# Kernel optimization log

Hardware: AMD Instinct MI355X
Metric: run time of the kernel (lower is better)

Reference implementation:

```python
import jax, jax.numpy as jnp
import numpy as np

N = 100000
E = 3200000
IN_DIM = 128
HID = 64
BN_EPS = 1e-5


def _gcn_conv(x, W, b, src, dst, dinv):
    h = x @ W                                      # [N, out]
    coeff = (dinv[src] * dinv[dst])[:, None]       # [E, 1]
    msg = h[src] * coeff                           # gather over edges
    agg = jax.ops.segment_sum(msg, dst, num_segments=N)
    agg = agg + h * (dinv * dinv)[:, None]         # self-loop term
    return agg + b


def setup_inputs() -> dict:
    key = jax.random.key(0)
    ks = jax.random.split(key, 12)
    x = jax.random.normal(ks[0], (N, IN_DIM), dtype=jnp.float32)
    edge_index = jax.random.randint(ks[1], (2, E), 0, N, dtype=jnp.int64)
    s1 = 1.0 / np.sqrt(IN_DIM)
    s2 = 1.0 / np.sqrt(HID)
    W1 = jax.random.uniform(ks[2], (IN_DIM, HID), jnp.float32, -s1, s1)
    b1 = jnp.zeros((HID,), jnp.float32)
    W2 = jax.random.uniform(ks[3], (HID, HID), jnp.float32, -s2, s2)
    b2 = jnp.zeros((HID,), jnp.float32)
    W3 = jax.random.uniform(ks[4], (HID, 1), jnp.float32, -s2, s2)
    b3 = jnp.zeros((1,), jnp.float32)
    g1 = jnp.ones((HID,), jnp.float32)
    beta1 = jnp.zeros((HID,), jnp.float32)
    m1 = 0.1 * jax.random.normal(ks[5], (HID,), jnp.float32)
    v1 = jax.random.uniform(ks[6], (HID,), jnp.float32) + 0.5
    g2 = jnp.ones((HID,), jnp.float32)
    beta2 = jnp.zeros((HID,), jnp.float32)
    m2 = 0.1 * jax.random.normal(ks[7], (HID,), jnp.float32)
    v2 = jax.random.uniform(ks[8], (HID,), jnp.float32) + 0.5
    return {"x": x, "edge_index": edge_index,
            "W1": W1, "b1": b1, "W2": W2, "b2": b2, "W3": W3, "b3": b3,
            "g1": g1, "beta1": beta1, "m1": m1, "v1": v1,
            "g2": g2, "beta2": beta2, "m2": m2, "v2": v2}


def reference(x, edge_index, W1, b1, W2, b2, W3, b3,
              g1, beta1, m1, v1, g2, beta2, m2, v2):
    src, dst = edge_index[0], edge_index[1]
    # degree with self-loops (computed on destination index, PyG convention)
    deg = jax.ops.segment_sum(jnp.ones((E,), jnp.float32), dst, num_segments=N) + 1.0
    dinv = jax.lax.rsqrt(deg)

    def bn(h, g, beta, m, v):
        return (h - m) * jax.lax.rsqrt(v + BN_EPS) * g + beta

    h = _gcn_conv(x, W1, b1, src, dst, dinv)
    h = jax.nn.relu(bn(h, g1, beta1, m1, v1))  # dropout is a no-op in eval
    h = _gcn_conv(h, W2, b2, src, dst, dinv)
    h = jax.nn.relu(bn(h, g2, beta2, m2, v2))
    h = _gcn_conv(h, W3, b3, src, dst, dinv)
    return jax.nn.sigmoid(h)  # [N, 1]
```

## Files before the change

kernel.cpp:

```cpp
#include <hip/hip_runtime.h>
#include <math.h>

#define N_NODES 100000
#define E_EDGES 3200000
#define IN_DIM_ 128
#define HID_ 64
#define BN_EPS_ 1e-5f

#define PB 250
#define CHUNK 12800
#define NBUCK 391
#define BMAX 9600

typedef __attribute__((ext_vector_type(8))) short short8;
typedef __attribute__((ext_vector_type(4))) float f32x4;
typedef __attribute__((ext_vector_type(2))) float f32x2;

__device__ inline ushort f2bf(float f) {
    union { float f; unsigned u; } c; c.f = f;
    unsigned r = c.u + 0x7fff + ((c.u >> 16) & 1);
    return (ushort)(r >> 16);
}
__device__ inline float bf_lo(unsigned p) { union { unsigned u; float f; } c; c.u = p << 16; return c.f; }
__device__ inline float bf_hi(unsigned p) { union { unsigned u; float f; } c; c.u = p & 0xffff0000u; return c.f; }
__device__ inline f32x2 up2(unsigned u) {
    union { unsigned u; float f; } lo, hi;
    lo.u = u << 16; hi.u = u & 0xffff0000u;
    f32x2 r; r.x = lo.f; r.y = hi.f; return r;
}

__global__ __launch_bounds__(512) void passA1_hist(const int* __restrict__ ei,
                                                   int* __restrict__ histPB) {
    __shared__ int hist[NBUCK];
    int t = threadIdx.x, b = blockIdx.x;
    for (int k = t; k < NBUCK; k += 512) hist[k] = 0;
    __syncthreads();
    int e0 = b * CHUNK, e1 = e0 + CHUNK;
    for (int e = e0 + t; e < e1; e += 512) {
        int d = ei[E_EDGES + e];
        atomicAdd(&hist[d >> 8], 1);
    }
    __syncthreads();
    for (int k = t; k < NBUCK; k += 512) histPB[k * PB + b] = hist[k];
}

__global__ __launch_bounds__(256) void scan_rows(int* __restrict__ histPB,
                                                 int* __restrict__ bucket_tot) {
    __shared__ int wsum[4];
    int k = blockIdx.x, t = threadIdx.x, lane = t & 63, wv = t >> 6;
    int v = (t < PB) ? histPB[k * PB + t] : 0;
    int s = v;
#pragma unroll
    for (int off = 1; off < 64; off <<= 1) {
        int u = __shfl_up(s, off, 64);
        if (lane >= off) s += u;
    }
    if (lane == 63) wsum[wv] = s;
    __syncthreads();
    int wbase = 0;
    for (int w = 0; w < wv; w++) wbase += wsum[w];
    if (t < PB) histPB[k * PB + t] = wbase + s - v;
    if (t == 255) bucket_tot[k] = wbase + s;
}

__global__ __launch_bounds__(512) void scan_totals(const int* __restrict__ bucket_tot,
                                                   int* __restrict__ bucket_base,
                                                   int* __restrict__ row_ptr) {
    __shared__ int wsum[8];
    int t = threadIdx.x, lane = t & 63, wv = t >> 6;
    int v = (t < NBUCK) ? bucket_tot[t] : 0;
    int s = v;
#pragma unroll
    for (int off = 1; off < 64; off <<= 1) {
        int u = __shfl_up(s, off, 64);
        if (lane >= off) s += u;
    }
    if (lane == 63) wsum[wv] = s;
    __syncthreads();
    int wbase = 0;
    for (int w = 0; w < wv; w++) wbase += wsum[w];
    if (t < NBUCK) bucket_base[t] = wbase + s - v;
    if (t == 0) {
        bucket_base[NBUCK] = E_EDGES;
        row_ptr[N_NODES] = E_EDGES;
    }
}

__global__ __launch_bounds__(512) void passA2_sorted(const int* __restrict__ ei,
                                                     const int* __restrict__ histPB,
                                                     const int* __restrict__ bucket_base,
                                                     int* __restrict__ ebuf) {
    __shared__ int sorted[CHUNK];
    __shared__ ushort bid[CHUNK];
    __shared__ int cur[NBUCK];
    __shared__ int lbase[NBUCK];
    int t = threadIdx.x, b = blockIdx.x;
    for (int k = t; k < NBUCK; k += 512) cur[k] = 0;
    __syncthreads();
    int e0 = b * CHUNK;
    for (int e = e0 + t; e < e0 + CHUNK; e += 512)
        atomicAdd(&cur[ei[E_EDGES + e] >> 8], 1);
    __syncthreads();
    if (t < 64) {
        int run = 0;
        for (int c0 = 0; c0 < NBUCK; c0 += 64) {
            int idx = c0 + t;
            int v = (idx < NBUCK) ? cur[idx] : 0;
            int s = v;
#pragma unroll
            for (int off = 1; off < 64; off <<= 1) {
                int u = __shfl_up(s, off, 64);
                if (t >= off) s += u;
            }
            if (idx < NBUCK) lbase[idx] = run + s - v;
            run += __shfl(s, 63, 64);
        }
    }
    __syncthreads();
    for (int k = t; k < NBUCK; k += 512) cur[k] = lbase[k];
    __syncthreads();
    for (int e = e0 + t; e < e0 + CHUNK; e += 512) {
        int s = ei[e];
        int d = ei[E_EDGES + e];
        int k = d >> 8;
        int pos = atomicAdd(&cur[k], 1);
        sorted[pos] = s | ((d & 255) << 17);
        bid[pos] = (ushort)k;
    }
    __syncthreads();
    for (int j = t; j < CHUNK; j += 512) {
        int k = bid[j];
        int dest = bucket_base[k] + histPB[k * PB + b] + (j - lbase[k]);
        ebuf[dest] = sorted[j];
    }
}

__global__ __launch_bounds__(256) void passB_sorted(const int* __restrict__ ebuf,
                                                    const int* __restrict__ bucket_base,
                                                    int* __restrict__ row_ptr,
                                                    int* __restrict__ csr_src,
                                                    float* __restrict__ dinv) {
    __shared__ int sorted[BMAX];
    __shared__ int hist[256];
    __shared__ int wsum[4];
    int b = blockIdx.x, t = threadIdx.x, lane = t & 63, wv = t >> 6;
    int base = bucket_base[b], end = bucket_base[b + 1];
    hist[t] = 0;
    __syncthreads();
    for (int k = base + t; k < end; k += 256)
        atomicAdd(&hist[ebuf[k] >> 17], 1);
    __syncthreads();
    int v = hist[t];
    int s = v;
#pragma unroll
    for (int off = 1; off < 64; off <<= 1) {
        int u = __shfl_up(s, off, 64);
        if (lane >= off) s += u;
    }
    if (lane == 63) wsum[wv] = s;
    __syncthreads();
    int wbase = 0;
    for (int w = 0; w < wv; w++) wbase += wsum[w];
    int excl = wbase + s - v;
    int node = b * 256 + t;
    if (node < N_NODES) {
        row_ptr[node] = base + excl;
        dinv[node] = rsqrtf((float)v + 1.0f);
    }
    __syncthreads();
    hist[t] = excl;
    __syncthreads();
    for (int k = base + t; k < end; k += 256) {
        int pv = ebuf[k];
        int pos = atomicAdd(&hist[pv >> 17], 1);
        if (pos < BMAX) sorted[pos] = pv;
        else csr_src[base + pos] = pv & 0x1FFFF;
    }
    __syncthreads();
    int cnt = end - base;
    if (cnt > BMAX) cnt = BMAX;
    for (int j = t; j < cnt; j += 256)
        csr_src[base + j] = sorted[j] & 0x1FFFF;
}

template<int K, bool BF16IN>
__global__ __launch_bounds__(256) void gemm_bf16(const void* __restrict__ Xv,
                                                 const float* __restrict__ W,
                                                 const float* __restrict__ dinv,
                                                 ushort* __restrict__ hs) {
    constexpr int KP = K + 8;
    __shared__ ushort A_lds[64][KP];
    __shared__ ushort Wt_lds[64][KP];
    int t = threadIdx.x;
    long row0 = (long)blockIdx.x * 64;

    for (int i = t; i < K * 16; i += 256) {
        float4 w4 = ((const float4*)W)[i];
        int k = i >> 4, n = (i & 15) * 4;
        Wt_lds[n + 0][k] = f2bf(w4.x);
        Wt_lds[n + 1][k] = f2bf(w4.y);
        Wt_lds[n + 2][k] = f2bf(w4.z);
        Wt_lds[n + 3][k] = f2bf(w4.w);
    }
    if (BF16IN) {
        constexpr int K2 = K / 2;
        const unsigned* X = (const unsigned*)Xv;
        for (int i = t; i < 64 * K2; i += 256) {
            int r = i / K2, c = i % K2;
            unsigned val = 0;
            long row = row0 + r;
            if (row < N_NODES) val = X[row * K2 + c];
            *(unsigned*)&A_lds[r][c * 2] = val;
        }
    } else {
        constexpr int K4 = K / 4;
        const float* X = (const float*)Xv;
        for (int i = t; i < 64 * K4; i += 256) {
            int r = i / K4, c = i % K4;
            float4 val = make_float4(0.f, 0.f, 0.f, 0.f);
            long row = row0 + r;
            if (row < N_NODES) val = ((const float4*)X)[row * K4 + c];
            int cb = c * 4;
            A_lds[r][cb + 0] = f2bf(val.x);
            A_lds[r][cb + 1] = f2bf(val.y);
            A_lds[r][cb + 2] = f2bf(val.z);
            A_lds[r][cb + 3] = f2bf(val.w);
        }
    }
    __syncthreads();

    int w = t >> 6, l = t & 63;
    int m = l & 15, quad = l >> 4;
    f32x4 acc[4];
#pragma unroll
    for (int c = 0; c < 4; c++) acc[c] = (f32x4){0.f, 0.f, 0.f, 0.f};

#pragma unroll
    for (int ch = 0; ch < K / 32; ch++) {
        short8 a = *(const short8*)&A_lds[16 * w + m][32 * ch + 8 * quad];
#pragma unroll
        for (int c = 0; c < 4; c++) {
            short8 b = *(const short8*)&Wt_lds[16 * c + m][32 * ch + 8 * quad];
            acc[c] = __builtin_amdgcn_mfma_f32_16x16x32_bf16(a, b, acc[c], 0, 0, 0);
        }
    }

#pragma unroll
    for (int r = 0; r < 4; r++) {
        long node = row0 + 16 * w + quad * 4 + r;
        if (node <= N_NODES) {
            float dv = (node < N_NODES) ? dinv[node] : 0.f;
#pragma unroll
            for (int c = 0; c < 4; c++)
                hs[node * 64 + 16 * c + m] = f2bf(acc[c][r] * dv);
        }
    }
}

template<bool LAST>
__global__ __launch_bounds__(256) void gather_feat(const int* __restrict__ row_ptr,
                                                   const int* __restrict__ csr_src,
                                                   const ushort* __restrict__ hs,
                                                   const float* __restrict__ dinv,
                                                   const float* __restrict__ b,
                                                   const float* __restrict__ g,
                                                   const float* __restrict__ beta,
                                                   const float* __restrict__ m,
                                                   const float* __restrict__ v,
                                                   unsigned* __restrict__ y,
                                                   const float* __restrict__ W3,
                                                   float* __restrict__ hs3, int n) {
    int i = (blockIdx.x * 256 + threadIdx.x) >> 6;
    if (i >= n) return;
    int l = threadIdx.x & 63;
    int es = l >> 3, fg = l & 7;
    const char* Hb = (const char*)hs;
    unsigned foff = (unsigned)fg << 4;
    unsigned zoff = ((unsigned)N_NODES << 7) + foff;

    f32x2 a01 = {0.f, 0.f}, a23 = {0.f, 0.f}, a45 = {0.f, 0.f}, a67 = {0.f, 0.f};

    if (es == 0) {
        uint4 p = *(const uint4*)(Hb + (((unsigned)i << 7) + foff));
        a01 += up2(p.x); a23 += up2(p.y); a45 += up2(p.z); a67 += up2(p.w);
    }

    int beg = row_ptr[i], end = row_ptr[i + 1];
    int endm1 = end - 1;
    for (int k = beg + es; k < end; k += 32) {
        int c1 = k + 8, c2 = k + 16, c3 = k + 24;
        int s0 = csr_src[k];
        int s1 = csr_src[c1 < end ? c1 : endm1];
        int s2 = csr_src[c2 < end ? c2 : endm1];
        int s3 = csr_src[c3 < end ? c3 : endm1];
        unsigned o0 = ((unsigned)s0 << 7) + foff;
        unsigned o1 = (c1 < end) ? (((unsigned)s1 << 7) + foff) : zoff;
        unsigned o2 = (c2 < end) ? (((unsigned)s2 << 7) + foff) : zoff;
        unsigned o3 = (c3 < end) ? (((unsigned)s3 << 7) + foff) : zoff;
        uint4 p0 = *(const uint4*)(Hb + o0);
        uint4 p1 = *(const uint4*)(Hb + o1);
        uint4 p2 = *(const uint4*)(Hb + o2);
        uint4 p3 = *(const uint4*)(Hb + o3);
        a01 += up2(p0.x); a23 += up2(p0.y); a45 += up2(p0.z); a67 += up2(p0.w);
        a01 += up2(p1.x); a23 += up2(p1.y); a45 += up2(p1.z); a67 += up2(p1.w);
        a01 += up2(p2.x); a23 += up2(p2.y); a45 += up2(p2.z); a67 += up2(p2.w);
        a01 += up2(p3.x); a23 += up2(p3.y); a45 += up2(p3.z); a67 += up2(p3.w);
    }

    float a0 = a01.x, a1 = a01.y, a2 = a23.x, a3 = a23.y;
    float a4 = a45.x, a5 = a45.y, a6 = a67.x, a7 = a67.y;

#pragma unroll
    for (int off = 8; off < 64; off <<= 1) {
        a0 += __shfl_xor(a0, off, 64);
        a1 += __shfl_xor(a1, off, 64);
        a2 += __shfl_xor(a2, off, 64);
        a3 += __shfl_xor(a3, off, 64);
        a4 += __shfl_xor(a4, off, 64);
        a5 += __shfl_xor(a5, off, 64);
        a6 += __shfl_xor(a6, off, 64);
        a7 += __shfl_xor(a7, off, 64);
    }

    float4 bb0 = ((const float4*)b)[fg * 2],    bb1 = ((const float4*)b)[fg * 2 + 1];
    float4 gg0 = ((const float4*)g)[fg * 2],    gg1 = ((const float4*)g)[fg * 2 + 1];
    float4 be0 = ((const float4*)beta)[fg * 2], be1 = ((const float4*)beta)[fg * 2 + 1];
    float4 mm0 = ((const float4*)m)[fg * 2],    mm1 = ((const float4*)m)[fg * 2 + 1];
    float4 vv0 = ((const float4*)v)[fg * 2],    vv1 = ((const float4*)v)[fg * 2 + 1];
    float di = dinv[i];
    float o0 = fmaxf((di * a0 + bb0.x - mm0.x) * (gg0.x * rsqrtf(vv0.x + BN_EPS_)) + be0.x, 0.f);
    float o1 = fmaxf((di * a1 + bb0.y - mm0.y) * (gg0.y * rsqrtf(vv0.y + BN_EPS_)) + be0.y, 0.f);
    float o2 = fmaxf((di * a2 + bb0.z - mm0.z) * (gg0.z * rsqrtf(vv0.z + BN_EPS_)) + be0.z, 0.f);
    float o3 = fmaxf((di * a3 + bb0.w - mm0.w) * (gg0.w * rsqrtf(vv0.w + BN_EPS_)) + be0.w, 0.f);
    float o4 = fmaxf((di * a4 + bb1.x - mm1.x) * (gg1.x * rsqrtf(vv1.x + BN_EPS_)) + be1.x, 0.f);
    float o5 = fmaxf((di * a5 + bb1.y - mm1.y) * (gg1.y * rsqrtf(vv1.y + BN_EPS_)) + be1.y, 0.f);
    float o6 = fmaxf((di * a6 + bb1.z - mm1.z) * (gg1.z * rsqrtf(vv1.z + BN_EPS_)) + be1.z, 0.f);
    float o7 = fmaxf((di * a7 + bb1.w - mm1.w) * (gg1.w * rsqrtf(vv1.w + BN_EPS_)) + be1.w, 0.f);

    if (LAST) {
        float4 w30 = ((const float4*)W3)[fg * 2], w31 = ((const float4*)W3)[fg * 2 + 1];
        float p = o0 * w30.x + o1 * w30.y + o2 * w30.z + o3 * w30.w +
                  o4 * w31.x + o5 * w31.y + o6 * w31.z + o7 * w31.w;
#pragma unroll
        for (int off = 1; off < 8; off <<= 1)
            p += __shfl_xor(p, off, 64);
        if (l == 0) hs3[i] = p * di;
    } else {
        if (es == 0) {
            uint4 pk;
            pk.x = (unsigned)f2bf(o0) | ((unsigned)f2bf(o1) << 16);
            pk.y = (unsigned)f2bf(o2) | ((unsigned)f2bf(o3) << 16);
            pk.z = (unsigned)f2bf(o4) | ((unsigned)f2bf(o5) << 16);
            pk.w = (unsigned)f2bf(o6) | ((unsigned)f2bf(o7) << 16);
            ((uint4*)y)[(long)i * 8 + fg] = pk;
        }
    }
}

__global__ __launch_bounds__(256) void gather3(const int* __restrict__ row_ptr,
                                               const int* __restrict__ csr_src,
                                               const float* __restrict__ hs3,
                                               const float* __restrict__ dinv,
                                               const float* __restrict__ b3,
                                               float* __restrict__ out, int n) {
    int i = blockIdx.x * 256 + threadIdx.x;
    if (i >= n) return;
    int beg = row_ptr[i], end = row_ptr[i + 1];
    float s0 = hs3[i], s1 = 0.f, s2 = 0.f, s3 = 0.f;
    float s4 = 0.f, s5 = 0.f, s6 = 0.f, s7 = 0.f;
    int k = beg;
    for (; k + 8 <= end; k += 8) {
        s0 += hs3[csr_src[k]];
        s1 += hs3[csr_src[k + 1]];
        s2 += hs3[csr_src[k + 2]];
        s3 += hs3[csr_src[k + 3]];
        s4 += hs3[csr_src[k + 4]];
        s5 += hs3[csr_src[k + 5]];
        s6 += hs3[csr_src[k + 6]];
        s7 += hs3[csr_src[k + 7]];
    }
    for (; k < end; k++) s0 += hs3[csr_src[k]];
    float z = dinv[i] * (((s0 + s1) + (s2 + s3)) + ((s4 + s5) + (s6 + s7))) + b3[0];
    out[i] = 1.f / (1.f + expf(-z));
}

extern "C" void kernel_launch(void* const* d_in, const int* in_sizes, int n_in,
                              void* d_out, int out_size, void* d_ws, size_t ws_size,
                              hipStream_t stream) {
    const int N = N_NODES;
    const int E = E_EDGES;

    const float* x   = (const float*)d_in[0];
    const int*   ei  = (const int*)d_in[1];
    const float* W1  = (const float*)d_in[2];
    const float* b1  = (const float*)d_in[3];
    const float* W2  = (const float*)d_in[4];
    const float* b2  = (const float*)d_in[5];
    const float* W3  = (const float*)d_in[6];
    const float* b3  = (const float*)d_in[7];
    const float* g1  = (const float*)d_in[8];
    const float* bt1 = (const float*)d_in[9];
    const float* m1  = (const float*)d_in[10];
    const float* v1  = (const float*)d_in[11];
    const float* g2  = (const float*)d_in[12];
    const float* bt2 = (const float*)d_in[13];
    const float* m2  = (const float*)d_in[14];
    const float* v2  = (const float*)d_in[15];
    float* out = (float*)d_out;

    int*    wsi         = (int*)d_ws;
    float*  dinv        = (float*)wsi;
    float*  hs3         = (float*)(wsi + (long)N);
    int*    row_ptr     = wsi + 2L * N;
    int*    histPB      = wsi + 3L * N + 16;
    int*    bucket_tot  = histPB + NBUCK * PB;
    int*    bucket_base = bucket_tot + 400;
    int*    csr_src     = bucket_base + 400;
    ushort* hsb         = (ushort*)(csr_src + (long)E);
    unsigned* yb        = (unsigned*)(csr_src + (long)E + 32L * (N + 1));
    int*    ebuf        = (int*)hsb;

    passA1_hist<<<PB, 512, 0, stream>>>(ei, histPB);
    scan_rows<<<NBUCK, 256, 0, stream>>>(histPB, bucket_tot);
    scan_totals<<<1, 512, 0, stream>>>(bucket_tot, bucket_base, row_ptr);
    passA2_sorted<<<PB, 512, 0, stream>>>(ei, histPB, bucket_base, ebuf);
    passB_sorted<<<NBUCK, 256, 0, stream>>>(ebuf, bucket_base, row_ptr, csr_src, dinv);

    gemm_bf16<IN_DIM_, false><<<(N + 63) / 64, 256, 0, stream>>>(x, W1, dinv, hsb);
    gather_feat<false><<<N / 4, 256, 0, stream>>>(row_ptr, csr_src, hsb, dinv,
                                                  b1, g1, bt1, m1, v1, yb, W3, hs3, N);
    gemm_bf16<HID_, true><<<(N + 63) / 64, 256, 0, stream>>>(yb, W2, dinv, hsb);
    gather_feat<true><<<N / 4, 256, 0, stream>>>(row_ptr, csr_src, hsb, dinv,
                                                 b2, g2, bt2, m2, v2, yb, W3, hs3, N);
    gather3<<<(N + 255) / 256, 256, 0, stream>>>(row_ptr, csr_src, hs3, dinv, b3, out, N);
}
```

Before: 397.5 us.

## Map eight rows per wave in gather and sort CSR neighbor lists per row

The feature gather now gives each group of 8 lanes its own destination row, so a wave handles 8 rows instead of one. Each lane group loops over its row's neighbors serially, 8 at a time, which removes the cross-lane shuffle reduction and the idle lanes on low-degree rows. A new bitonic sort kernel orders each row's source indices (for degree up to 64) to improve locality of the gathered rows. The cost is an extra kernel launch and sort pass, plus divergence between rows of different degree inside a wave.

```diff
diff --git a/kernel.cpp b/kernel.cpp
--- a/kernel.cpp
+++ b/kernel.cpp
@@ -21,8 +21,6 @@
     unsigned r = c.u + 0x7fff + ((c.u >> 16) & 1);
     return (ushort)(r >> 16);
 }
-__device__ inline float bf_lo(unsigned p) { union { unsigned u; float f; } c; c.u = p << 16; return c.f; }
-__device__ inline float bf_hi(unsigned p) { union { unsigned u; float f; } c; c.u = p & 0xffff0000u; return c.f; }
 __device__ inline f32x2 up2(unsigned u) {
     union { unsigned u; float f; } lo, hi;
     lo.u = u << 16; hi.u = u & 0xffff0000u;
@@ -181,6 +179,119 @@
     if (cnt > BMAX) cnt = BMAX;
     for (int j = t; j < cnt; j += 256)
         csr_src[base + j] = sorted[j] & 0x1FFFF;
+}
+
+__global__ __launch_bounds__(256) void sort_rows(const int* __restrict__ row_ptr,
+                                                 int* __restrict__ csr_src) {
+    int wv = (blockIdx.x * 256 + threadIdx.x) >> 6;
+    int lane = threadIdx.x & 63;
+    if (wv >= N_NODES) return;
+    int beg = row_ptr[wv], end = row_ptr[wv + 1];
+    int deg = end - beg;
+    if (deg <= 1 || deg > 64) return;
+    int val = (lane < deg) ? csr_src[beg + lane] : 0x7FFFFFFF;
+#pragma unroll
+    for (int k = 2; k <= 64; k <<= 1) {
+#pragma unroll
+        for (int j = 32; j > 0; j >>= 1) {
+            if (j >= k) continue;
+            int other = __shfl_xor(val, j, 64);
+            bool lower = (lane & j) == 0;
+            bool asc = (lane & k) == 0;
+            int mn = min(val, other), mx = max(val, other);
+            val = (lower == asc) ? mn : mx;
+        }
+    }
+    if (lane < deg) csr_src[beg + lane] = val;
+}
+
+template<bool LAST>
+__global__ __launch_bounds__(256) void gather_feat(const int* __restrict__ row_ptr,
+                                                   const int* __restrict__ csr_src,
+                                                   const ushort* __restrict__ hs,
+                                                   const float* __restrict__ dinv,
+                                                   const float* __restrict__ b,
+                                                   const float* __restrict__ g,
+                                                   const float* __restrict__ beta,
+                                                   const float* __restrict__ m,
+                                                   const float* __restrict__ v,
+                                                   unsigned* __restrict__ y,
+                                                   const float* __restrict__ W3,
+                                                   float* __restrict__ hs3, int n) {
+    int wave = (blockIdx.x * 256 + threadIdx.x) >> 6;
+    if ((wave << 3) >= n) return;
+    int l = threadIdx.x & 63;
+    int es = l >> 3, fg = l & 7;
+    int i = (wave << 3) + es;
+    bool rowok = i < n;
+    int ic = rowok ? i : (n - 1);
+
+    const char* Hb = (const char*)hs;
+    unsigned foff = (unsigned)fg << 4;
+    unsigned zoff = ((unsigned)N_NODES << 7) + foff;
+
+    f32x2 a01 = {0.f, 0.f}, a23 = {0.f, 0.f}, a45 = {0.f, 0.f}, a67 = {0.f, 0.f};
+
+    {
+        uint4 p = *(const uint4*)(Hb + (((unsigned)ic << 7) + foff));
+        a01 += up2(p.x); a23 += up2(p.y); a45 += up2(p.z); a67 += up2(p.w);
+    }
+
+    int beg = row_ptr[ic], end = row_ptr[ic + 1];
+    for (int k = beg; k < end; k += 8) {
+        unsigned o[8];
+#pragma unroll
+        for (int j = 0; j < 8; j++) {
+            int kj = k + j;
+            int sj = csr_src[kj < end ? kj : k];
+            o[j] = (kj < end) ? (((unsigned)sj << 7) + foff) : zoff;
+        }
+        uint4 p[8];
+#pragma unroll
+        for (int j = 0; j < 8; j++) p[j] = *(const uint4*)(Hb + o[j]);
+#pragma unroll
+        for (int j = 0; j < 8; j++) {
+            a01 += up2(p[j].x); a23 += up2(p[j].y);
+            a45 += up2(p[j].z); a67 += up2(p[j].w);
+        }
+    }
+
+    float a0 = a01.x, a1 = a01.y, a2 = a23.x, a3 = a23.y;
+    float a4 = a45.x, a5 = a45.y, a6 = a67.x, a7 = a67.y;
+
+    float4 bb0 = ((const float4*)b)[fg * 2],    bb1 = ((const float4*)b)[fg * 2 + 1];
+    float4 gg0 = ((const float4*)g)[fg * 2],    gg1 = ((const float4*)g)[fg * 2 + 1];
+    float4 be0 = ((const float4*)beta)[fg * 2], be1 = ((const float4*)beta)[fg * 2 + 1];
+    float4 mm0 = ((const float4*)m)[fg * 2],    mm1 = ((const float4*)m)[fg * 2 + 1];
+    float4 vv0 = ((const float4*)v)[fg * 2],    vv1 = ((const float4*)v)[fg * 2 + 1];
+    float di = dinv[ic];
+    float o0 = fmaxf((di * a0 + bb0.x - mm0.x) * (gg0.x * rsqrtf(vv0.x + BN_EPS_)) + be0.x, 0.f);
+    float o1 = fmaxf((di * a1 + bb0.y - mm0.y) * (gg0.y * rsqrtf(vv0.y + BN_EPS_)) + be0.y, 0.f);
+    float o2 = fmaxf((di * a2 + bb0.z - mm0.z) * (gg0.z * rsqrtf(vv0.z + BN_EPS_)) + be0.z, 0.f);
+    float o3 = fmaxf((di * a3 + bb0.w - mm0.w) * (gg0.w * rsqrtf(vv0.w + BN_EPS_)) + be0.w, 0.f);
+    float o4 = fmaxf((di * a4 + bb1.x - mm1.x) * (gg1.x * rsqrtf(vv1.x + BN_EPS_)) + be1.x, 0.f);
+    float o5 = fmaxf((di * a5 + bb1.y - mm1.y) * (gg1.y * rsqrtf(vv1.y + BN_EPS_)) + be1.y, 0.f);
+    float o6 = fmaxf((di * a6 + bb1.z - mm1.z) * (gg1.z * rsqrtf(vv1.z + BN_EPS_)) + be1.z, 0.f);
+    float o7 = fmaxf((di * a7 + bb1.w - mm1.w) * (gg1.w * rsqrtf(vv1.w + BN_EPS_)) + be1.w, 0.f);
+
+    if (LAST) {
+        float4 w30 = ((const float4*)W3)[fg * 2], w31 = ((const float4*)W3)[fg * 2 + 1];
+        float p = o0 * w30.x + o1 * w30.y + o2 * w30.z + o3 * w30.w +
+                  o4 * w31.x + o5 * w31.y + o6 * w31.z + o7 * w31.w;
+#pragma unroll
+        for (int off = 1; off < 8; off <<= 1)
+            p += __shfl_xor(p, off, 64);
+        if (fg == 0 && rowok) hs3[i] = p * di;
+    } else {
+        if (rowok) {
+            uint4 pk;
+            pk.x = (unsigned)f2bf(o0) | ((unsigned)f2bf(o1) << 16);
+            pk.y = (unsigned)f2bf(o2) | ((unsigned)f2bf(o3) << 16);
+            pk.z = (unsigned)f2bf(o4) | ((unsigned)f2bf(o5) << 16);
+            pk.w = (unsigned)f2bf(o6) | ((unsigned)f2bf(o7) << 16);
+            ((uint4*)y)[(long)i * 8 + fg] = pk;
+        }
+    }
 }
 
 template<int K, bool BF16IN>
@@ -253,106 +364,6 @@
 #pragma unroll
             for (int c = 0; c < 4; c++)
                 hs[node * 64 + 16 * c + m] = f2bf(acc[c][r] * dv);
-        }
-    }
-}
-
-template<bool LAST>
-__global__ __launch_bounds__(256) void gather_feat(const int* __restrict__ row_ptr,
-                                                   const int* __restrict__ csr_src,
-                                                   const ushort* __restrict__ hs,
-                                                   const float* __restrict__ dinv,
-                                                   const float* __restrict__ b,
-                                                   const float* __restrict__ g,
-                                                   const float* __restrict__ beta,
-                                                   const float* __restrict__ m,
-                                                   const float* __restrict__ v,
-                                                   unsigned* __restrict__ y,
-                                                   const float* __restrict__ W3,
-                                                   float* __restrict__ hs3, int n) {
-    int i = (blockIdx.x * 256 + threadIdx.x) >> 6;
-    if (i >= n) return;
-    int l = threadIdx.x & 63;
-    int es = l >> 3, fg = l & 7;
-    const char* Hb = (const char*)hs;
-    unsigned foff = (unsigned)fg << 4;
-    unsigned zoff = ((unsigned)N_NODES << 7) + foff;
-
-    f32x2 a01 = {0.f, 0.f}, a23 = {0.f, 0.f}, a45 = {0.f, 0.f}, a67 = {0.f, 0.f};
-
-    if (es == 0) {
-        uint4 p = *(const uint4*)(Hb + (((unsigned)i << 7) + foff));
-        a01 += up2(p.x); a23 += up2(p.y); a45 += up2(p.z); a67 += up2(p.w);
-    }
-
-    int beg = row_ptr[i], end = row_ptr[i + 1];
-    int endm1 = end - 1;
-    for (int k = beg + es; k < end; k += 32) {
-        int c1 = k + 8, c2 = k + 16, c3 = k + 24;
-        int s0 = csr_src[k];
-        int s1 = csr_src[c1 < end ? c1 : endm1];
-        int s2 = csr_src[c2 < end ? c2 : endm1];
-        int s3 = csr_src[c3 < end ? c3 : endm1];
-        unsigned o0 = ((unsigned)s0 << 7) + foff;
-        unsigned o1 = (c1 < end) ? (((unsigned)s1 << 7) + foff) : zoff;
-        unsigned o2 = (c2 < end) ? (((unsigned)s2 << 7) + foff) : zoff;
-        unsigned o3 = (c3 < end) ? (((unsigned)s3 << 7) + foff) : zoff;
-        uint4 p0 = *(const uint4*)(Hb + o0);
-        uint4 p1 = *(const uint4*)(Hb + o1);
-        uint4 p2 = *(const uint4*)(Hb + o2);
-        uint4 p3 = *(const uint4*)(Hb + o3);
-        a01 += up2(p0.x); a23 += up2(p0.y); a45 += up2(p0.z); a67 += up2(p0.w);
-        a01 += up2(p1.x); a23 += up2(p1.y); a45 += up2(p1.z); a67 += up2(p1.w);
-        a01 += up2(p2.x); a23 += up2(p2.y); a45 += up2(p2.z); a67 += up2(p2.w);
-        a01 += up2(p3.x); a23 += up2(p3.y); a45 += up2(p3.z); a67 += up2(p3.w);
-    }
-
-    float a0 = a01.x, a1 = a01.y, a2 = a23.x, a3 = a23.y;
-    float a4 = a45.x, a5 = a45.y, a6 = a67.x, a7 = a67.y;
-
-#pragma unroll
-    for (int off = 8; off < 64; off <<= 1) {
-        a0 += __shfl_xor(a0, off, 64);
-        a1 += __shfl_xor(a1, off, 64);
-        a2 += __shfl_xor(a2, off, 64);
-        a3 += __shfl_xor(a3, off, 64);
-        a4 += __shfl_xor(a4, off, 64);
-        a5 += __shfl_xor(a5, off, 64);
-        a6 += __shfl_xor(a6, off, 64);
-        a7 += __shfl_xor(a7, off, 64);
-    }
-
-    float4 bb0 = ((const float4*)b)[fg * 2],    bb1 = ((const float4*)b)[fg * 2 + 1];
-    float4 gg0 = ((const float4*)g)[fg * 2],    gg1 = ((const float4*)g)[fg * 2 + 1];
-    float4 be0 = ((const float4*)beta)[fg * 2], be1 = ((const float4*)beta)[fg * 2 + 1];
-    float4 mm0 = ((const float4*)m)[fg * 2],    mm1 = ((const float4*)m)[fg * 2 + 1];
-    float4 vv0 = ((const float4*)v)[fg * 2],    vv1 = ((const float4*)v)[fg * 2 + 1];
-    float di = dinv[i];
-    float o0 = fmaxf((di * a0 + bb0.x - mm0.x) * (gg0.x * rsqrtf(vv0.x + BN_EPS_)) + be0.x, 0.f);
-    float o1 = fmaxf((di * a1 + bb0.y - mm0.y) * (gg0.y * rsqrtf(vv0.y + BN_EPS_)) + be0.y, 0.f);
-    float o2 = fmaxf((di * a2 + bb0.z - mm0.z) * (gg0.z * rsqrtf(vv0.z + BN_EPS_)) + be0.z, 0.f);
-    float o3 = fmaxf((di * a3 + bb0.w - mm0.w) * (gg0.w * rsqrtf(vv0.w + BN_EPS_)) + be0.w, 0.f);
-    float o4 = fmaxf((di * a4 + bb1.x - mm1.x) * (gg1.x * rsqrtf(vv1.x + BN_EPS_)) + be1.x, 0.f);
-    float o5 = fmaxf((di * a5 + bb1.y - mm1.y) * (gg1.y * rsqrtf(vv1.y + BN_EPS_)) + be1.y, 0.f);
-    float o6 = fmaxf((di * a6 + bb1.z - mm1.z) * (gg1.z * rsqrtf(vv1.z + BN_EPS_)) + be1.z, 0.f);
-    float o7 = fmaxf((di * a7 + bb1.w - mm1.w) * (gg1.w * rsqrtf(vv1.w + BN_EPS_)) + be1.w, 0.f);
-
-    if (LAST) {
-        float4 w30 = ((const float4*)W3)[fg * 2], w31 = ((const float4*)W3)[fg * 2 + 1];
-        float p = o0 * w30.x + o1 * w30.y + o2 * w30.z + o3 * w30.w +
-                  o4 * w31.x + o5 * w31.y + o6 * w31.z + o7 * w31.w;
-#pragma unroll
-        for (int off = 1; off < 8; off <<= 1)
-            p += __shfl_xor(p, off, 64);
-        if (l == 0) hs3[i] = p * di;
-    } else {
-        if (es == 0) {
-            uint4 pk;
-            pk.x = (unsigned)f2bf(o0) | ((unsigned)f2bf(o1) << 16);
-            pk.y = (unsigned)f2bf(o2) | ((unsigned)f2bf(o3) << 16);
-            pk.z = (unsigned)f2bf(o4) | ((unsigned)f2bf(o5) << 16);
-            pk.w = (unsigned)f2bf(o6) | ((unsigned)f2bf(o7) << 16);
-            ((uint4*)y)[(long)i * 8 + fg] = pk;
         }
     }
 }
@@ -425,12 +436,13 @@
     scan_totals<<<1, 512, 0, stream>>>(bucket_tot, bucket_base, row_ptr);
     passA2_sorted<<<PB, 512, 0, stream>>>(ei, histPB, bucket_base, ebuf);
     passB_sorted<<<NBUCK, 256, 0, stream>>>(ebuf, bucket_base, row_ptr, csr_src, dinv);
+    sort_rows<<<(N + 3) / 4, 256, 0, stream>>>(row_ptr, csr_src);
 
     gemm_bf16<IN_DIM_, false><<<(N + 63) / 64, 256, 0, stream>>>(x, W1, dinv, hsb);
-    gather_feat<false><<<N / 4, 256, 0, stream>>>(row_ptr, csr_src, hsb, dinv,
-                                                  b1, g1, bt1, m1, v1, yb, W3, hs3, N);
+    gather_feat<false><<<(N + 31) / 32, 256, 0, stream>>>(row_ptr, csr_src, hsb, dinv,
+                                                          b1, g1, bt1, m1, v1, yb, W3, hs3, N);
     gemm_bf16<HID_, true><<<(N + 63) / 64, 256, 0, stream>>>(yb, W2, dinv, hsb);
-    gather_feat<true><<<N / 4, 256, 0, stream>>>(row_ptr, csr_src, hsb, dinv,
-                                                 b2, g2, bt2, m2, v2, yb, W3, hs3, N);
+    gather_feat<true><<<(N + 31) / 32, 256, 0, stream>>>(row_ptr, csr_src, hsb, dinv,
+                                                         b2, g2, bt2, m2, v2, yb, W3, hs3, N);
     gather3<<<(N + 255) / 256, 256, 0, stream>>>(row_ptr, csr_src, hs3, dinv, b3, out, N);
 }
```

After: 409.3 us. 3.0% more time.

## Split gather into four feature-slice passes over padded CSR rows

Applied to the files above, without the earlier changes.

The hidden features are stored as four column slices of 16 bf16 values each, and each aggregation runs as four separate gather kernels, one per slice. Each slice table (about 3.2 MB) is small enough to stay in cache during the random neighbour gathers. CSR rows are padded to multiples of 8 with a dummy zero node, which removes bounds checks and tail loops. Node degrees now come from a separate global atomic histogram, adding kernels and per-slice launch overhead plus 32-byte-granular gathers that may waste bandwidth.

```diff
diff --git a/kernel.cpp b/kernel.cpp
--- a/kernel.cpp
+++ b/kernel.cpp
@@ -11,6 +11,7 @@
 #define CHUNK 12800
 #define NBUCK 391
 #define BMAX 9600
+#define SUB (N_NODES + 1)
 
 typedef __attribute__((ext_vector_type(8))) short short8;
 typedef __attribute__((ext_vector_type(4))) float f32x4;
@@ -21,8 +22,6 @@
     unsigned r = c.u + 0x7fff + ((c.u >> 16) & 1);
     return (ushort)(r >> 16);
 }
-__device__ inline float bf_lo(unsigned p) { union { unsigned u; float f; } c; c.u = p << 16; return c.f; }
-__device__ inline float bf_hi(unsigned p) { union { unsigned u; float f; } c; c.u = p & 0xffff0000u; return c.f; }
 __device__ inline f32x2 up2(unsigned u) {
     union { unsigned u; float f; } lo, hi;
     lo.u = u << 16; hi.u = u & 0xffff0000u;
@@ -30,9 +29,12 @@
 }
 
 __global__ __launch_bounds__(512) void passA1_hist(const int* __restrict__ ei,
-                                                   int* __restrict__ histPB) {
+                                                   int* __restrict__ histPB,
+                                                   int* __restrict__ deg) {
     __shared__ int hist[NBUCK];
     int t = threadIdx.x, b = blockIdx.x;
+    int g = b * 512 + t;
+    if (g < N_NODES) deg[g] = 0;
     for (int k = t; k < NBUCK; k += 512) hist[k] = 0;
     __syncthreads();
     int e0 = b * CHUNK, e1 = e0 + CHUNK;
@@ -42,6 +44,13 @@
     }
     __syncthreads();
     for (int k = t; k < NBUCK; k += 512) histPB[k * PB + b] = hist[k];
+}
+
+__global__ __launch_bounds__(256) void deg_hist(const int* __restrict__ ei,
+                                                int* __restrict__ deg) {
+    int stride = gridDim.x * 256;
+    for (int e = blockIdx.x * 256 + threadIdx.x; e < E_EDGES; e += stride)
+        atomicAdd(&deg[ei[E_EDGES + e]], 1);
 }
 
 __global__ __launch_bounds__(256) void scan_rows(int* __restrict__ histPB,
@@ -63,26 +72,51 @@
     if (t == 255) bucket_tot[k] = wbase + s;
 }
 
-__global__ __launch_bounds__(512) void scan_totals(const int* __restrict__ bucket_tot,
-                                                   int* __restrict__ bucket_base,
-                                                   int* __restrict__ row_ptr) {
-    __shared__ int wsum[8];
+__global__ __launch_bounds__(256) void pad_tot_k(const int* __restrict__ deg,
+                                                 int* __restrict__ bucket_ptot,
+                                                 float* __restrict__ dinv) {
+    __shared__ int wsum[4];
+    int b = blockIdx.x, t = threadIdx.x, lane = t & 63, wv = t >> 6;
+    int node = b * 256 + t;
+    int d = (node < N_NODES) ? deg[node] : 0;
+    if (node < N_NODES) dinv[node] = rsqrtf((float)d + 1.0f);
+    int pd = (d + 7) & ~7;
+#pragma unroll
+    for (int off = 1; off < 64; off <<= 1) pd += __shfl_xor(pd, off, 64);
+    if (lane == 0) wsum[wv] = pd;
+    __syncthreads();
+    if (t == 0) bucket_ptot[b] = wsum[0] + wsum[1] + wsum[2] + wsum[3];
+}
+
+__global__ __launch_bounds__(512) void scan_totals2(const int* __restrict__ bucket_tot,
+                                                    const int* __restrict__ bucket_ptot,
+                                                    int* __restrict__ bucket_base,
+                                                    int* __restrict__ bucket_pbase,
+                                                    int* __restrict__ row_ptr,
+                                                    float* __restrict__ hs3) {
+    __shared__ int wsA[8], wsB[8];
     int t = threadIdx.x, lane = t & 63, wv = t >> 6;
-    int v = (t < NBUCK) ? bucket_tot[t] : 0;
-    int s = v;
+    int va = (t < NBUCK) ? bucket_tot[t] : 0;
+    int vb = (t < NBUCK) ? bucket_ptot[t] : 0;
+    int sa = va, sb = vb;
 #pragma unroll
     for (int off = 1; off < 64; off <<= 1) {
-        int u = __shfl_up(s, off, 64);
-        if (lane >= off) s += u;
-    }
-    if (lane == 63) wsum[wv] = s;
-    __syncthreads();
-    int wbase = 0;
-    for (int w = 0; w < wv; w++) wbase += wsum[w];
-    if (t < NBUCK) bucket_base[t] = wbase + s - v;
+        int ua = __shfl_up(sa, off, 64);
+        int ub = __shfl_up(sb, off, 64);
+        if (lane >= off) { sa += ua; sb += ub; }
+    }
+    if (lane == 63) { wsA[wv] = sa; wsB[wv] = sb; }
+    __syncthreads();
+    int wa = 0, wb = 0;
+    for (int w = 0; w < wv; w++) { wa += wsA[w]; wb += wsB[w]; }
+    if (t < NBUCK) {
+        bucket_base[t]  = wa + sa - va;
+        bucket_pbase[t] = wb + sb - vb;
+    }
+    if (t == NBUCK - 1) row_ptr[N_NODES] = wb + sb;
     if (t == 0) {
         bucket_base[NBUCK] = E_EDGES;
-        row_ptr[N_NODES] = E_EDGES;
+        hs3[N_NODES] = 0.f;
     }
 }
 
@@ -137,128 +171,54 @@
 
 __global__ __launch_bounds__(256) void passB_sorted(const int* __restrict__ ebuf,
                                                     const int* __restrict__ bucket_base,
+                                                    const int* __restrict__ bucket_pbase,
+                                                    const int* __restrict__ deg,
                                                     int* __restrict__ row_ptr,
-                                                    int* __restrict__ csr_src,
-                                                    float* __restrict__ dinv) {
+                                                    int* __restrict__ csr_src) {
     __shared__ int sorted[BMAX];
-    __shared__ int hist[256];
-    __shared__ int wsum[4];
+    __shared__ int ucur[256];
+    __shared__ int ubeg[256];
+    __shared__ int pbeg[256];
+    __shared__ int wsA[4], wsB[4];
     int b = blockIdx.x, t = threadIdx.x, lane = t & 63, wv = t >> 6;
     int base = bucket_base[b], end = bucket_base[b + 1];
-    hist[t] = 0;
-    __syncthreads();
-    for (int k = base + t; k < end; k += 256)
-        atomicAdd(&hist[ebuf[k] >> 17], 1);
-    __syncthreads();
-    int v = hist[t];
-    int s = v;
+    int pbase = bucket_pbase[b];
+    int node = b * 256 + t;
+    int d = (node < N_NODES) ? deg[node] : 0;
+    int pd = (d + 7) & ~7;
+    int sa = d, sb = pd;
 #pragma unroll
     for (int off = 1; off < 64; off <<= 1) {
-        int u = __shfl_up(s, off, 64);
-        if (lane >= off) s += u;
-    }
-    if (lane == 63) wsum[wv] = s;
-    __syncthreads();
-    int wbase = 0;
-    for (int w = 0; w < wv; w++) wbase += wsum[w];
-    int excl = wbase + s - v;
-    int node = b * 256 + t;
-    if (node < N_NODES) {
-        row_ptr[node] = base + excl;
-        dinv[node] = rsqrtf((float)v + 1.0f);
-    }
-    __syncthreads();
-    hist[t] = excl;
+        int ua = __shfl_up(sa, off, 64);
+        int ub = __shfl_up(sb, off, 64);
+        if (lane >= off) { sa += ua; sb += ub; }
+    }
+    if (lane == 63) { wsA[wv] = sa; wsB[wv] = sb; }
+    __syncthreads();
+    int wa = 0, wb = 0;
+    for (int w = 0; w < wv; w++) { wa += wsA[w]; wb += wsB[w]; }
+    int uex = wa + sa - d, pex = wb + sb - pd;
+    ubeg[t] = uex; pbeg[t] = pex; ucur[t] = uex;
+    if (node < N_NODES) row_ptr[node] = pbase + pex;
     __syncthreads();
     for (int k = base + t; k < end; k += 256) {
         int pv = ebuf[k];
-        int pos = atomicAdd(&hist[pv >> 17], 1);
+        int pos = atomicAdd(&ucur[pv >> 17], 1);
         if (pos < BMAX) sorted[pos] = pv;
-        else csr_src[base + pos] = pv & 0x1FFFF;
-    }
-    __syncthreads();
-    int cnt = end - base;
-    if (cnt > BMAX) cnt = BMAX;
-    for (int j = t; j < cnt; j += 256)
-        csr_src[base + j] = sorted[j] & 0x1FFFF;
-}
-
-template<int K, bool BF16IN>
-__global__ __launch_bounds__(256) void gemm_bf16(const void* __restrict__ Xv,
-                                                 const float* __restrict__ W,
-                                                 const float* __restrict__ dinv,
-                                                 ushort* __restrict__ hs) {
-    constexpr int KP = K + 8;
-    __shared__ ushort A_lds[64][KP];
-    __shared__ ushort Wt_lds[64][KP];
-    int t = threadIdx.x;
-    long row0 = (long)blockIdx.x * 64;
-
-    for (int i = t; i < K * 16; i += 256) {
-        float4 w4 = ((const float4*)W)[i];
-        int k = i >> 4, n = (i & 15) * 4;
-        Wt_lds[n + 0][k] = f2bf(w4.x);
-        Wt_lds[n + 1][k] = f2bf(w4.y);
-        Wt_lds[n + 2][k] = f2bf(w4.z);
-        Wt_lds[n + 3][k] = f2bf(w4.w);
-    }
-    if (BF16IN) {
-        constexpr int K2 = K / 2;
-        const unsigned* X = (const unsigned*)Xv;
-        for (int i = t; i < 64 * K2; i += 256) {
-            int r = i / K2, c = i % K2;
-            unsigned val = 0;
-            long row = row0 + r;
-            if (row < N_NODES) val = X[row * K2 + c];
-            *(unsigned*)&A_lds[r][c * 2] = val;
-        }
-    } else {
-        constexpr int K4 = K / 4;
-        const float* X = (const float*)Xv;
-        for (int i = t; i < 64 * K4; i += 256) {
-            int r = i / K4, c = i % K4;
-            float4 val = make_float4(0.f, 0.f, 0.f, 0.f);
-            long row = row0 + r;
-            if (row < N_NODES) val = ((const float4*)X)[row * K4 + c];
-            int cb = c * 4;
-            A_lds[r][cb + 0] = f2bf(val.x);
-            A_lds[r][cb + 1] = f2bf(val.y);
-            A_lds[r][cb + 2] = f2bf(val.z);
-            A_lds[r][cb + 3] = f2bf(val.w);
-        }
-    }
-    __syncthreads();
-
-    int w = t >> 6, l = t & 63;
-    int m = l & 15, quad = l >> 4;
-    f32x4 acc[4];
-#pragma unroll
-    for (int c = 0; c < 4; c++) acc[c] = (f32x4){0.f, 0.f, 0.f, 0.f};
-
-#pragma unroll
-    for (int ch = 0; ch < K / 32; ch++) {
-        short8 a = *(const short8*)&A_lds[16 * w + m][32 * ch + 8 * quad];
-#pragma unroll
-        for (int c = 0; c < 4; c++) {
-            short8 b = *(const short8*)&Wt_lds[16 * c + m][32 * ch + 8 * quad];
-            acc[c] = __builtin_amdgcn_mfma_f32_16x16x32_bf16(a, b, acc[c], 0, 0, 0);
-        }
-    }
-
-#pragma unroll
-    for (int r = 0; r < 4; r++) {
-        long node = row0 + 16 * w + quad * 4 + r;
-        if (node <= N_NODES) {
-            float dv = (node < N_NODES) ? dinv[node] : 0.f;
-#pragma unroll
-            for (int c = 0; c < 4; c++)
-                hs[node * 64 + 16 * c + m] = f2bf(acc[c][r] * dv);
-        }
-    }
-}
-
-template<bool LAST>
-__global__ __launch_bounds__(256) void gather_feat(const int* __restrict__ row_ptr,
+    }
+    __syncthreads();
+    for (int r = wv; r < 256; r += 4) {
+        int nd = b * 256 + r;
+        int d2 = (nd < N_NODES) ? deg[nd] : 0;
+        int pd2 = (d2 + 7) & ~7;
+        int ub = ubeg[r], pb = pbeg[r];
+        for (int c = lane; c < pd2; c += 64)
+            csr_src[pbase + pb + c] = (c < d2) ? (sorted[ub + c] & 0x1FFFF) : N_NODES;
+    }
+}
+
+template<bool LAST, int P>
+__global__ __launch_bounds__(256) void gather_pass(const int* __restrict__ row_ptr,
                                                    const int* __restrict__ csr_src,
                                                    const ushort* __restrict__ hs,
                                                    const float* __restrict__ dinv,
@@ -274,85 +234,134 @@
     if (i >= n) return;
     int l = threadIdx.x & 63;
     int es = l >> 3, fg = l & 7;
-    const char* Hb = (const char*)hs;
-    unsigned foff = (unsigned)fg << 4;
-    unsigned zoff = ((unsigned)N_NODES << 7) + foff;
-
-    f32x2 a01 = {0.f, 0.f}, a23 = {0.f, 0.f}, a45 = {0.f, 0.f}, a67 = {0.f, 0.f};
-
-    if (es == 0) {
-        uint4 p = *(const uint4*)(Hb + (((unsigned)i << 7) + foff));
-        a01 += up2(p.x); a23 += up2(p.y); a45 += up2(p.z); a67 += up2(p.w);
-    }
-
-    int beg = row_ptr[i], end = row_ptr[i + 1];
-    int endm1 = end - 1;
-    for (int k = beg + es; k < end; k += 32) {
-        int c1 = k + 8, c2 = k + 16, c3 = k + 24;
-        int s0 = csr_src[k];
-        int s1 = csr_src[c1 < end ? c1 : endm1];
-        int s2 = csr_src[c2 < end ? c2 : endm1];
-        int s3 = csr_src[c3 < end ? c3 : endm1];
-        unsigned o0 = ((unsigned)s0 << 7) + foff;
-        unsigned o1 = (c1 < end) ? (((unsigned)s1 << 7) + foff) : zoff;
-        unsigned o2 = (c2 < end) ? (((unsigned)s2 << 7) + foff) : zoff;
-        unsigned o3 = (c3 < end) ? (((unsigned)s3 << 7) + foff) : zoff;
-        uint4 p0 = *(const uint4*)(Hb + o0);
-        uint4 p1 = *(const uint4*)(Hb + o1);
-        uint4 p2 = *(const uint4*)(Hb + o2);
-        uint4 p3 = *(const uint4*)(Hb + o3);
-        a01 += up2(p0.x); a23 += up2(p0.y); a45 += up2(p0.z); a67 += up2(p0.w);
-        a01 += up2(p1.x); a23 += up2(p1.y); a45 += up2(p1.z); a67 += up2(p1.w);
-        a01 += up2(p2.x); a23 += up2(p2.y); a45 += up2(p2.z); a67 += up2(p2.w);
-        a01 += up2(p3.x); a23 += up2(p3.y); a45 += up2(p3.z); a67 += up2(p3.w);
-    }
-
-    float a0 = a01.x, a1 = a01.y, a2 = a23.x, a3 = a23.y;
-    float a4 = a45.x, a5 = a45.y, a6 = a67.x, a7 = a67.y;
+
+    const unsigned* T = (const unsigned*)hs + (long)P * SUB * 8;
+
+    f32x2 acc = {0.f, 0.f};
+    if (es == 0) acc += up2(T[(unsigned)i * 8 + fg]);
+
+    int pbeg = row_ptr[i], pend = row_ptr[i + 1];
+    const int* cs = csr_src + pbeg;
+    int nb8 = (pend - pbeg) >> 3;
+    int k = es;
+    int full = nb8 >> 2;
+    for (int t = 0; t < full; t++, k += 32) {
+        int s0 = cs[k], s1 = cs[k + 8], s2 = cs[k + 16], s3 = cs[k + 24];
+        unsigned u0 = T[(unsigned)s0 * 8 + fg];
+        unsigned u1 = T[(unsigned)s1 * 8 + fg];
+        unsigned u2 = T[(unsigned)s2 * 8 + fg];
+        unsigned u3 = T[(unsigned)s3 * 8 + fg];
+        acc += up2(u0); acc += up2(u1); acc += up2(u2); acc += up2(u3);
+    }
+    for (int rem = nb8 & 3; rem > 0; rem--, k += 8) {
+        int s = cs[k];
+        acc += up2(T[(unsigned)s * 8 + fg]);
+    }
 
 #pragma unroll
     for (int off = 8; off < 64; off <<= 1) {
-        a0 += __shfl_xor(a0, off, 64);
-        a1 += __shfl_xor(a1, off, 64);
-        a2 += __shfl_xor(a2, off, 64);
-        a3 += __shfl_xor(a3, off, 64);
-        a4 += __shfl_xor(a4, off, 64);
-        a5 += __shfl_xor(a5, off, 64);
-        a6 += __shfl_xor(a6, off, 64);
-        a7 += __shfl_xor(a7, off, 64);
-    }
-
-    float4 bb0 = ((const float4*)b)[fg * 2],    bb1 = ((const float4*)b)[fg * 2 + 1];
-    float4 gg0 = ((const float4*)g)[fg * 2],    gg1 = ((const float4*)g)[fg * 2 + 1];
-    float4 be0 = ((const float4*)beta)[fg * 2], be1 = ((const float4*)beta)[fg * 2 + 1];
-    float4 mm0 = ((const float4*)m)[fg * 2],    mm1 = ((const float4*)m)[fg * 2 + 1];
-    float4 vv0 = ((const float4*)v)[fg * 2],    vv1 = ((const float4*)v)[fg * 2 + 1];
+        acc.x += __shfl_xor(acc.x, off, 64);
+        acc.y += __shfl_xor(acc.y, off, 64);
+    }
+
+    float2 bb = ((const float2*)b)[P * 8 + fg];
+    float2 gg = ((const float2*)g)[P * 8 + fg];
+    float2 be = ((const float2*)beta)[P * 8 + fg];
+    float2 mm = ((const float2*)m)[P * 8 + fg];
+    float2 vv = ((const float2*)v)[P * 8 + fg];
     float di = dinv[i];
-    float o0 = fmaxf((di * a0 + bb0.x - mm0.x) * (gg0.x * rsqrtf(vv0.x + BN_EPS_)) + be0.x, 0.f);
-    float o1 = fmaxf((di * a1 + bb0.y - mm0.y) * (gg0.y * rsqrtf(vv0.y + BN_EPS_)) + be0.y, 0.f);
-    float o2 = fmaxf((di * a2 + bb0.z - mm0.z) * (gg0.z * rsqrtf(vv0.z + BN_EPS_)) + be0.z, 0.f);
-    float o3 = fmaxf((di * a3 + bb0.w - mm0.w) * (gg0.w * rsqrtf(vv0.w + BN_EPS_)) + be0.w, 0.f);
-    float o4 = fmaxf((di * a4 + bb1.x - mm1.x) * (gg1.x * rsqrtf(vv1.x + BN_EPS_)) + be1.x, 0.f);
-    float o5 = fmaxf((di * a5 + bb1.y - mm1.y) * (gg1.y * rsqrtf(vv1.y + BN_EPS_)) + be1.y, 0.f);
-    float o6 = fmaxf((di * a6 + bb1.z - mm1.z) * (gg1.z * rsqrtf(vv1.z + BN_EPS_)) + be1.z, 0.f);
-    float o7 = fmaxf((di * a7 + bb1.w - mm1.w) * (gg1.w * rsqrtf(vv1.w + BN_EPS_)) + be1.w, 0.f);
+    float o0 = fmaxf((di * acc.x + bb.x - mm.x) * (gg.x * rsqrtf(vv.x + BN_EPS_)) + be.x, 0.f);
+    float o1 = fmaxf((di * acc.y + bb.y - mm.y) * (gg.y * rsqrtf(vv.y + BN_EPS_)) + be.y, 0.f);
 
     if (LAST) {
-        float4 w30 = ((const float4*)W3)[fg * 2], w31 = ((const float4*)W3)[fg * 2 + 1];
-        float p = o0 * w30.x + o1 * w30.y + o2 * w30.z + o3 * w30.w +
-                  o4 * w31.x + o5 * w31.y + o6 * w31.z + o7 * w31.w;
+        float2 w3 = ((const float2*)W3)[P * 8 + fg];
+        float p = o0 * w3.x + o1 * w3.y;
 #pragma unroll
         for (int off = 1; off < 8; off <<= 1)
             p += __shfl_xor(p, off, 64);
-        if (l == 0) hs3[i] = p * di;
+        if (l == 0) {
+            float prev = (P == 0) ? 0.f : hs3[i];
+            float now = prev + p;
+            hs3[i] = (P == 3) ? now * di : now;
+        }
     } else {
         if (es == 0) {
-            uint4 pk;
-            pk.x = (unsigned)f2bf(o0) | ((unsigned)f2bf(o1) << 16);
-            pk.y = (unsigned)f2bf(o2) | ((unsigned)f2bf(o3) << 16);
-            pk.z = (unsigned)f2bf(o4) | ((unsigned)f2bf(o5) << 16);
-            pk.w = (unsigned)f2bf(o6) | ((unsigned)f2bf(o7) << 16);
-            ((uint4*)y)[(long)i * 8 + fg] = pk;
+            unsigned pk = (unsigned)f2bf(o0) | ((unsigned)f2bf(o1) << 16);
+            y[(unsigned)i * 32 + P * 8 + fg] = pk;
+        }
+    }
+}
+
+template<int K, bool BF16IN>
+__global__ __launch_bounds__(256) void gemm_bf16(const void* __restrict__ Xv,
+                                                 const float* __restrict__ W,
+                                                 const float* __restrict__ dinv,
+                                                 ushort* __restrict__ hs) {
+    constexpr int KP = K + 8;
+    __shared__ ushort A_lds[64][KP];
+    __shared__ ushort Wt_lds[64][KP];
+    int t = threadIdx.x;
+    long row0 = (long)blockIdx.x * 64;
+
+    for (int i = t; i < K * 16; i += 256) {
+        float4 w4 = ((const float4*)W)[i];
+        int k = i >> 4, n = (i & 15) * 4;
+        Wt_lds[n + 0][k] = f2bf(w4.x);
+        Wt_lds[n + 1][k] = f2bf(w4.y);
+        Wt_lds[n + 2][k] = f2bf(w4.z);
+        Wt_lds[n + 3][k] = f2bf(w4.w);
+    }
+    if (BF16IN) {
+        constexpr int K2 = K / 2;
+        const unsigned* X = (const unsigned*)Xv;
+        for (int i = t; i < 64 * K2; i += 256) {
+            int r = i / K2, c = i % K2;
+            unsigned val = 0;
+            long row = row0 + r;
+            if (row < N_NODES) val = X[row * K2 + c];
+            *(unsigned*)&A_lds[r][c * 2] = val;
+        }
+    } else {
+        constexpr int K4 = K / 4;
+        const float* X = (const float*)Xv;
+        for (int i = t; i < 64 * K4; i += 256) {
+            int r = i / K4, c = i % K4;
+            float4 val = make_float4(0.f, 0.f, 0.f, 0.f);
+            long row = row0 + r;
+            if (row < N_NODES) val = ((const float4*)X)[row * K4 + c];
+            int cb = c * 4;
+            A_lds[r][cb + 0] = f2bf(val.x);
+            A_lds[r][cb + 1] = f2bf(val.y);
+            A_lds[r][cb + 2] = f2bf(val.z);
+            A_lds[r][cb + 3] = f2bf(val.w);
+        }
+    }
+    __syncthreads();
+
+    int w = t >> 6, l = t & 63;
+    int m = l & 15, quad = l >> 4;
+    f32x4 acc[4];
+#pragma unroll
+    for (int c = 0; c < 4; c++) acc[c] = (f32x4){0.f, 0.f, 0.f, 0.f};
+
+#pragma unroll
+    for (int ch = 0; ch < K / 32; ch++) {
+        short8 a = *(const short8*)&A_lds[16 * w + m][32 * ch + 8 * quad];
+#pragma unroll
+        for (int c = 0; c < 4; c++) {
+            short8 b = *(const short8*)&Wt_lds[16 * c + m][32 * ch + 8 * quad];
+            acc[c] = __builtin_amdgcn_mfma_f32_16x16x32_bf16(a, b, acc[c], 0, 0, 0);
+        }
+    }
+
+#pragma unroll
+    for (int r = 0; r < 4; r++) {
+        long node = row0 + 16 * w + quad * 4 + r;
+        if (node <= N_NODES) {
+            float dv = (node < N_NODES) ? dinv[node] : 0.f;
+#pragma unroll
+            for (int c = 0; c < 4; c++)
+                hs[((long)c * SUB + node) * 16 + m] = f2bf(acc[c][r] * dv);
         }
     }
 }
@@ -368,8 +377,7 @@
     int beg = row_ptr[i], end = row_ptr[i + 1];
     float s0 = hs3[i], s1 = 0.f, s2 = 0.f, s3 = 0.f;
     float s4 = 0.f, s5 = 0.f, s6 = 0.f, s7 = 0.f;
-    int k = beg;
-    for (; k + 8 <= end; k += 8) {
+    for (int k = beg; k + 8 <= end; k += 8) {
         s0 += hs3[csr_src[k]];
         s1 += hs3[csr_src[k + 1]];
         s2 += hs3[csr_src[k + 2]];
@@ -379,7 +387,6 @@
         s6 += hs3[csr_src[k + 6]];
         s7 += hs3[csr_src[k + 7]];
     }
-    for (; k < end; k++) s0 += hs3[csr_src[k]];
     float z = dinv[i] * (((s0 + s1) + (s2 + s3)) + ((s4 + s5) + (s6 + s7))) + b3[0];
     out[i] = 1.f / (1.f + expf(-z));
 }
@@ -388,7 +395,6 @@
                               void* d_out, int out_size, void* d_ws, size_t ws_size,
                               hipStream_t stream) {
     const int N = N_NODES;
-    const int E = E_EDGES;
 
     const float* x   = (const float*)d_in[0];
     const int*   ei  = (const int*)d_in[1];
@@ -408,29 +414,50 @@
     const float* v2  = (const float*)d_in[15];
     float* out = (float*)d_out;
 
-    int*    wsi         = (int*)d_ws;
-    float*  dinv        = (float*)wsi;
-    float*  hs3         = (float*)(wsi + (long)N);
-    int*    row_ptr     = wsi + 2L * N;
-    int*    histPB      = wsi + 3L * N + 16;
-    int*    bucket_tot  = histPB + NBUCK * PB;
-    int*    bucket_base = bucket_tot + 400;
-    int*    csr_src     = bucket_base + 400;
-    ushort* hsb         = (ushort*)(csr_src + (long)E);
-    unsigned* yb        = (unsigned*)(csr_src + (long)E + 32L * (N + 1));
-    int*    ebuf        = (int*)hsb;
-
-    passA1_hist<<<PB, 512, 0, stream>>>(ei, histPB);
+    int*    wsi          = (int*)d_ws;
+    float*  dinv         = (float*)wsi;
+    float*  hs3          = (float*)(wsi + (long)N);
+    int*    row_ptr      = wsi + 2L * N + 16;
+    int*    deg          = row_ptr + N + 16;
+    int*    histPB       = deg + N + 16;
+    int*    bucket_tot   = histPB + NBUCK * PB;
+    int*    bucket_base  = bucket_tot + 400;
+    int*    bucket_ptot  = bucket_base + 400;
+    int*    bucket_pbase = bucket_ptot + 400;
+    ushort* hsb          = (ushort*)(bucket_pbase + 402);
+    unsigned* yb         = (unsigned*)((int*)(void*)hsb + 32L * SUB);
+    int*    csr_src      = (int*)yb + 32L * N;
+    int*    ebuf         = (int*)(void*)hsb;
+
+    passA1_hist<<<PB, 512, 0, stream>>>(ei, histPB, deg);
+    deg_hist<<<1024, 256, 0, stream>>>(ei, deg);
     scan_rows<<<NBUCK, 256, 0, stream>>>(histPB, bucket_tot);
-    scan_totals<<<1, 512, 0, stream>>>(bucket_tot, bucket_base, row_ptr);
+    pad_tot_k<<<NBUCK, 256, 0, stream>>>(deg, bucket_ptot, dinv);
+    scan_totals2<<<1, 512, 0, stream>>>(bucket_tot, bucket_ptot, bucket_base,
+                                        bucket_pbase, row_ptr, hs3);
     passA2_sorted<<<PB, 512, 0, stream>>>(ei, histPB, bucket_base, ebuf);
-    passB_sorted<<<NBUCK, 256, 0, stream>>>(ebuf, bucket_base, row_ptr, csr_src, dinv);
+    passB_sorted<<<NBUCK, 256, 0, stream>>>(ebuf, bucket_base, bucket_pbase,
+                                            deg, row_ptr, csr_src);
+
+    const int GG = (N + 3) / 4;
 
     gemm_bf16<IN_DIM_, false><<<(N + 63) / 64, 256, 0, stream>>>(x, W1, dinv, hsb);
-    gather_feat<false><<<N / 4, 256, 0, stream>>>(row_ptr, csr_src, hsb, dinv,
+    gather_pass<false, 0><<<GG, 256, 0, stream>>>(row_ptr, csr_src, hsb, dinv,
+                                                  b1, g1, bt1, m1, v1, yb, W3, hs3, N);
+    gather_pass<false, 1><<<GG, 256, 0, stream>>>(row_ptr, csr_src, hsb, dinv,
+                                                  b1, g1, bt1, m1, v1, yb, W3, hs3, N);
+    gather_pass<false, 2><<<GG, 256, 0, stream>>>(row_ptr, csr_src, hsb, dinv,
+                                                  b1, g1, bt1, m1, v1, yb, W3, hs3, N);
+    gather_pass<false, 3><<<GG, 256, 0, stream>>>(row_ptr, csr_src, hsb, dinv,
                                                   b1, g1, bt1, m1, v1, yb, W3, hs3, N);
     gemm_bf16<HID_, true><<<(N + 63) / 64, 256, 0, stream>>>(yb, W2, dinv, hsb);
-    gather_feat<true><<<N / 4, 256, 0, stream>>>(row_ptr, csr_src, hsb, dinv,
+    gather_pass<true, 0><<<GG, 256, 0, stream>>>(row_ptr, csr_src, hsb, dinv,
+                                                 b2, g2, bt2, m2, v2, yb, W3, hs3, N);
+    gather_pass<true, 1><<<GG, 256, 0, stream>>>(row_ptr, csr_src, hsb, dinv,
+                                                 b2, g2, bt2, m2, v2, yb, W3, hs3, N);
+    gather_pass<true, 2><<<GG, 256, 0, stream>>>(row_ptr, csr_src, hsb, dinv,
+                                                 b2, g2, bt2, m2, v2, yb, W3, hs3, N);
+    gather_pass<true, 3><<<GG, 256, 0, stream>>>(row_ptr, csr_src, hsb, dinv,
                                                  b2, g2, bt2, m2, v2, yb, W3, hs3, N);
     gather3<<<(N + 255) / 256, 256, 0, stream>>>(row_ptr, csr_src, hs3, dinv, b3, out, N);
 }
```

After: 716.3 us. +80.2%, slower.
